# Kernel tuning notes

Measured on AMD Instinct MI355X. Metric: run time of the kernel, lower is better.

Reference implementation:

```python
import jax, jax.numpy as jnp
import numpy as np

B, T, E, H = 32, 256, 512, 512


def setup_inputs() -> dict:
    key = jax.random.key(0)
    ks = jax.random.split(key, 9)
    s_e = 1.0 / np.sqrt(E)  # nn.Linear default init bound
    s_h = 1.0 / np.sqrt(H)

    def u(k, shape, s):
        return jax.random.uniform(k, shape, jnp.float32, -s, s)

    # Gate order along the 4H axis: [in, forget, cell, out]
    return {
        "x": jax.random.normal(ks[0], (B, T, E), jnp.float32),
        "fwd_Wih": u(ks[1], (E, 4 * H), s_e),
        "fwd_bih": u(ks[2], (4 * H,), s_e),
        "fwd_Whh": u(ks[3], (H, 4 * H), s_h),
        "fwd_bhh": u(ks[4], (4 * H,), s_h),
        "bwd_Wih": u(ks[5], (E, 4 * H), s_e),
        "bwd_bih": u(ks[6], (4 * H,), s_e),
        "bwd_Whh": u(ks[7], (H, 4 * H), s_h),
        "bwd_bhh": u(ks[8], (4 * H,), s_h),
    }


def _lstm(x_seq, Wih, bih, Whh, bhh):
    """Run one LSTM direction over x_seq [B,T,E]; returns hidden states [B,T,H]
    in scan order (no flipping), matching the torch loop."""
    b, h = x_seq.shape[0], Whh.shape[0]
    # Precompute all input projections (and fold both biases) in one big GEMM.
    xg = jnp.einsum("bte,eg->tbg", x_seq, Wih) + bih + bhh  # [T,B,4H]
    h0 = jnp.zeros((b, h), x_seq.dtype)
    c0 = jnp.zeros((b, h), x_seq.dtype)

    def step(carry, xg_t):
        hprev, cprev = carry
        g = xg_t + hprev @ Whh  # [B,4H]
        i, f, gc, o = jnp.split(g, 4, axis=-1)
        c = jax.nn.sigmoid(f) * cprev + jax.nn.sigmoid(i) * jnp.tanh(gc)
        hnew = jax.nn.sigmoid(o) * jnp.tanh(c)
        return (hnew, c), hnew

    _, hs = jax.lax.scan(step, (h0, c0), xg)  # hs: [T,B,H]
    return hs.transpose(1, 0, 2)


def reference(x, fwd_Wih, fwd_bih, fwd_Whh, fwd_bhh,
              bwd_Wih, bwd_bih, bwd_Whh, bwd_bhh):
    fwd = _lstm(x, fwd_Wih, fwd_bih, fwd_Whh, fwd_bhh)
    # Backward direction processes reversed inputs; outputs are stacked in
    # processing order (the torch module does NOT re-flip them).
    bwd = _lstm(x[:, ::-1, :], bwd_Wih, bwd_bih, bwd_Whh, bwd_bhh)
    return jnp.concatenate([fwd, bwd], axis=-1)  # [B,T,2H]
```

## Files before the change

kernel.cpp:

```cpp
#include <hip/hip_runtime.h>
#include <hip/hip_bf16.h>
#include <math.h>

static constexpr int BB = 32;
static constexpr int TT = 256;
static constexpr int EE = 512;
static constexpr int HH = 512;
static constexpr int GG = 2048;

static constexpr int HS2 = 12;

using u16 = unsigned short;

__device__ __forceinline__ float bf2f(u16 u) {
    return __uint_as_float(((unsigned int)u) << 16);
}
__device__ __forceinline__ u16 f2bf(float f) {
    unsigned int u = __float_as_uint(f);
    unsigned int r = 0x7FFFu + ((u >> 16) & 1u);
    return (u16)((u + r) >> 16);
}
__device__ __forceinline__ float sigm(float x) {
    return 1.0f / (1.0f + expf(-x));
}

__device__ __forceinline__ float4 ld_b128_sc(const float4* p) {
    float4 v;
    asm volatile("global_load_dwordx4 %0, %1, off sc0 sc1" : "=v"(v) : "v"(p));
    return v;
}
__device__ __forceinline__ void st_b32_sc(float* p, float v) {
    asm volatile("global_store_dword %0, %1, off sc0 sc1" :: "v"(p), "v"(v) : "memory");
}

template<bool F32>
__device__ __forceinline__ float ldw(const void* p, size_t i) {
    if constexpr (F32) return ((const float*)p)[i];
    else               return bf2f(((const u16*)p)[i]);
}
template<bool F32>
__device__ __forceinline__ float4 ld4(const void* p, size_t i) {
    if constexpr (F32) {
        return *(const float4*)((const float*)p + i);
    } else {
        ushort4 v = *(const ushort4*)((const u16*)p + i);
        return make_float4(bf2f(v.x), bf2f(v.y), bf2f(v.z), bf2f(v.w));
    }
}

__global__ void init_state(const u16* __restrict__ bih_probe,
                           float* __restrict__ h_st, float* __restrict__ c_st,
                           int* __restrict__ bar, int* __restrict__ flag) {
    size_t i = (size_t)blockIdx.x * blockDim.x + threadIdx.x;
    size_t stride = (size_t)gridDim.x * blockDim.x;
    for (size_t j = i; j < (size_t)2*2*BB*HH; j += stride) h_st[j] = 0.0f;
    for (size_t j = i; j < (size_t)2*BB*HH;   j += stride) c_st[j] = 0.0f;
    for (size_t j = i; j < 1024;              j += stride) bar[j] = 0;
    if (blockIdx.x == 0 && threadIdx.x == 0) {
        int f = 0;
        for (int k = 0; k < 2048; ++k) {
            int e = (bih_probe[k] >> 7) & 0xFF;
            if (e >= 127) f = 1;
        }
        *flag = f;
    }
}

template<bool F32>
__device__ __forceinline__ void xg_body(
    const void* __restrict__ x, const void* __restrict__ Wih,
    const void* __restrict__ bih, const void* __restrict__ bhh,
    float* __restrict__ xgp, int d, int mt, int nt, float* b_lds)
{
    const int tid = threadIdx.x;
    const int tn = tid & 15;
    const int tm = tid >> 4;
    const int m0 = mt * 64;
    const int n0 = nt * 64;

    size_t a_off[4];
    #pragma unroll
    for (int i = 0; i < 4; ++i) {
        const int m = m0 + 4*tm + i;
        const int t = m >> 5, b = m & 31;
        const int t_src = d ? (TT - 1 - t) : t;
        a_off[i] = ((size_t)b * TT + t_src) * EE;
    }

    float acc[4][4];
    #pragma unroll
    for (int i = 0; i < 4; ++i)
        #pragma unroll
        for (int j = 0; j < 4; ++j) acc[i][j] = 0.0f;

    const int kr = tid >> 2;
    const int nc = (tid & 3) * 16;

    for (int k0 = 0; k0 < EE; k0 += 64) {
        __syncthreads();
        #pragma unroll 4
        for (int e = 0; e < 16; ++e)
            b_lds[kr*64 + nc + e] = ldw<F32>(Wih, (size_t)(k0 + kr)*GG + n0 + nc + e);
        __syncthreads();

        #pragma unroll 2
        for (int kk = 0; kk < 64; kk += 4) {
            float4 av[4];
            #pragma unroll
            for (int i = 0; i < 4; ++i) av[i] = ld4<F32>(x, a_off[i] + k0 + kk);
            #pragma unroll
            for (int j = 0; j < 4; ++j) {
                const float4 bv = *(const float4*)&b_lds[(kk + j)*64 + 4*tn];
                #pragma unroll
                for (int i = 0; i < 4; ++i) {
                    const float a = (j == 0) ? av[i].x : (j == 1) ? av[i].y
                                  : (j == 2) ? av[i].z : av[i].w;
                    acc[i][0] += a * bv.x; acc[i][1] += a * bv.y;
                    acc[i][2] += a * bv.z; acc[i][3] += a * bv.w;
                }
            }
        }
    }

    const int mbase = m0 + 4*tm;
    const int tt = mbase >> 5, bb = mbase & 31;
    #pragma unroll
    for (int j = 0; j < 4; ++j) {
        const int col  = n0 + 4*tn + j;
        const float bs = ldw<F32>(bih, col) + ldw<F32>(bhh, col);
        const int g    = col >> 9;
        const int hc   = col & 511;
        const int wgc  = hc >> 4;
        const int hcl  = hc & 15;
        const int bg8  = bb >> 3;
        const int brem = bb & 7;
        const size_t idx = (((size_t)d*TT + tt)*65536)
                         + (size_t)bg8*16384 + (size_t)wgc*512
                         + (size_t)(hcl*4 + g)*8 + brem;
        float4 v = make_float4(acc[0][j] + bs, acc[1][j] + bs,
                               acc[2][j] + bs, acc[3][j] + bs);
        *(float4*)&xgp[idx] = v;
    }
}

__global__ __launch_bounds__(256) void xg_gemm(
    const void* __restrict__ x,
    const void* __restrict__ WihF, const void* __restrict__ bihF, const void* __restrict__ bhhF,
    const void* __restrict__ WihB, const void* __restrict__ bihB, const void* __restrict__ bhhB,
    float* __restrict__ xgp, const int* __restrict__ flag)
{
    __shared__ float b_lds[64 * 64];
    const int bid = blockIdx.x;
    const int d  = bid >> 12;
    const int r  = bid & 4095;
    const int mt = r >> 5;
    const int nt = r & 31;
    const void* Wih = d ? WihB : WihF;
    const void* bih = d ? bihB : bihF;
    const void* bhh = d ? bhhB : bhhF;
    if (*flag) xg_body<true >(x, Wih, bih, bhh, xgp, d, mt, nt, b_lds);
    else       xg_body<false>(x, Wih, bih, bhh, xgp, d, mt, nt, b_lds);
}

template<bool F32>
__device__ __forceinline__ void rec_body(
    const void* __restrict__ Whh,
    const float* __restrict__ xgp,
    float* __restrict__ hT,
    int* __restrict__ bar,
    void* __restrict__ out, int d, int bg8, int wgc,
    float* __restrict__ w_lds,
    float* __restrict__ h_lds,
    float* __restrict__ gbuf)
{
    const int tid = threadIdx.x;
    const int kg = tid & 7;
    const int bq = (tid >> 3) & 1;
    const int cq = tid >> 4;

    {
        const int c  = tid & 63;
        const int kq = tid >> 6;
        const int gcol = (c & 3)*512 + wgc*16 + (c >> 2);
        char* wb = (char*)w_lds;
        for (int k = kq*128; k < kq*128 + 128; ++k) {
            const unsigned byte = (unsigned)(k*256 + c*4) ^ ((unsigned)(k & 7) << 4);
            *(float*)(wb + byte) = ldw<F32>(Whh, (size_t)k*GG + gcol);
        }
    }

    const int ch = d*4 + bg8;
    int* barc = bar + ch*128;
    float* hTc = hT + (size_t)ch * 8192;

    float cr = 0.0f;
    const int ghcl = tid >> 3;
    const int gb   = tid & 7;

    const char* wpB = (const char*)w_lds + kg*256 + ((unsigned)(cq*16) ^ ((unsigned)kg << 4));
    const float* hp = h_lds + kg*HS2 + bq*4;

    __syncthreads();

    for (int t = 0; t < TT; ++t) {
        const int parity = t & 1;
        const float4* hprev4 = (const float4*)(hTc + (parity ^ 1) * 4096);
        float*        hnext  = hTc + parity * 4096;

        float xgv[4] = {0.f, 0.f, 0.f, 0.f};
        if (tid < 128) {
            const float* xgs = xgp + (((size_t)d*TT + t)*65536)
                             + (size_t)bg8*16384 + (size_t)wgc*512;
            #pragma unroll
            for (int g = 0; g < 4; ++g)
                xgv[g] = xgs[(ghcl*4 + g)*8 + gb];
        }

        float4 hstg[4];
        #pragma unroll
        for (int i = 0; i < 4; ++i)
            hstg[i] = ld_b128_sc(hprev4 + i*256 + tid);
        asm volatile("s_waitcnt vmcnt(0)" ::: "memory");
        __builtin_amdgcn_sched_barrier(0);
        #pragma unroll
        for (int i = 0; i < 4; ++i) {
            const int idx = i*256 + tid;
            const int k  = idx >> 1;
            const int b4 = idx & 1;
            *(float4*)&h_lds[k*HS2 + b4*4] = hstg[i];
        }
        __syncthreads();

        float acc[4][4];
        #pragma unroll
        for (int i = 0; i < 4; ++i)
            #pragma unroll
            for (int j = 0; j < 4; ++j) acc[i][j] = 0.0f;
        #pragma unroll 8
        for (int kk = 0; kk < 64; ++kk) {
            const float4 wv = *(const float4*)(wpB + kk*2048);
            const float4 hv = *(const float4*)(hp + kk*(8*HS2));
            acc[0][0] += wv.x*hv.x; acc[0][1] += wv.x*hv.y; acc[0][2] += wv.x*hv.z; acc[0][3] += wv.x*hv.w;
            acc[1][0] += wv.y*hv.x; acc[1][1] += wv.y*hv.y; acc[1][2] += wv.y*hv.z; acc[1][3] += wv.y*hv.w;
            acc[2][0] += wv.z*hv.x; acc[2][1] += wv.z*hv.y; acc[2][2] += wv.z*hv.z; acc[2][3] += wv.z*hv.w;
            acc[3][0] += wv.w*hv.x; acc[3][1] += wv.w*hv.y; acc[3][2] += wv.w*hv.z; acc[3][3] += wv.w*hv.w;
        }

        #pragma unroll
        for (int i = 0; i < 4; ++i)
            #pragma unroll
            for (int j = 0; j < 4; ++j) {
                float v = acc[i][j];
                v += __shfl_xor(v, 1);
                v += __shfl_xor(v, 2);
                v += __shfl_xor(v, 4);
                acc[i][j] = v;
            }
        if (kg < 4) {
            const int ci = kg;
            *(float4*)&gbuf[(cq*4 + ci)*8 + bq*4] =
                make_float4(acc[ci][0], acc[ci][1], acc[ci][2], acc[ci][3]);
        }
        __syncthreads();

        if (tid < 128) {
            const float gi = gbuf[(ghcl*4 + 0)*8 + gb] + xgv[0];
            const float gf = gbuf[(ghcl*4 + 1)*8 + gb] + xgv[1];
            const float gc = gbuf[(ghcl*4 + 2)*8 + gb] + xgv[2];
            const float go = gbuf[(ghcl*4 + 3)*8 + gb] + xgv[3];
            const float cn = sigm(gf)*cr + sigm(gi)*tanhf(gc);
            cr = cn;
            const float hv = sigm(go)*tanhf(cn);
            const int hc = wgc*16 + ghcl;
            st_b32_sc(hnext + (size_t)hc*8 + gb, hv);
            const int bglob = bg8*8 + gb;
            const size_t oi = ((size_t)bglob*TT + t)*(2*HH) + (size_t)d*HH + hc;
            if constexpr (F32) ((float*)out)[oi] = hv;
            else               ((u16*)out)[oi]   = f2bf(hv);
        }

        asm volatile("s_waitcnt vmcnt(0)" ::: "memory");
        __syncthreads();
        if (tid == 0) {
            __hip_atomic_fetch_add(barc, 1, __ATOMIC_RELAXED, __HIP_MEMORY_SCOPE_AGENT);
            const int tgt = 32 * (t + 1);
            while (__hip_atomic_load(barc, __ATOMIC_RELAXED, __HIP_MEMORY_SCOPE_AGENT) < tgt)
                __builtin_amdgcn_s_sleep(1);
        }
        __syncthreads();
    }
}

__global__ __launch_bounds__(256, 1) void lstm_rec(
    const void* __restrict__ WhhF, const void* __restrict__ WhhB,
    const float* __restrict__ xgp, float* __restrict__ hT,
    int* __restrict__ bar, const int* __restrict__ flag,
    void* __restrict__ out)
{
    __shared__ float w_lds[512 * 64];
    __shared__ float h_lds[512 * HS2];
    __shared__ float gbuf[512];
    const int wg  = blockIdx.x;
    const int d   = wg >> 7;
    const int r   = wg & 127;
    const int bg8 = r >> 5;
    const int wgc = r & 31;
    const void* Whh = d ? WhhB : WhhF;
    if (*flag) rec_body<true >(Whh, xgp, hT, bar, out, d, bg8, wgc, w_lds, h_lds, gbuf);
    else       rec_body<false>(Whh, xgp, hT, bar, out, d, bg8, wgc, w_lds, h_lds, gbuf);
}

template<bool F32>
__device__ __forceinline__ void step_body(
    const void* __restrict__ x,
    const void* __restrict__ Wih, const void* __restrict__ bih,
    const void* __restrict__ Whh, const void* __restrict__ bhh,
    const float* __restrict__ h_prev, float* __restrict__ h_next,
    float* __restrict__ c_st, void* __restrict__ out,
    int d, int nblk, int t, int t_src, float* __restrict__ gbuf)
{
    const int tid = threadIdx.x;
    const int c0  = tid & 15;
    const int g   = c0 >> 2;
    const int nl  = c0 & 3;
    const int bq  = tid >> 4;
    const int col = g*512 + nblk*4 + nl;
    const int b0 = bq*2, b1 = b0 + 1;

    float p00=0.f,p01=0.f,p02=0.f,p03=0.f;
    float p10=0.f,p11=0.f,p12=0.f,p13=0.f;
    {
        const size_t xo0 = ((size_t)b0*TT + t_src) * EE;
        const size_t xo1 = ((size_t)b1*TT + t_src) * EE;
        #pragma unroll 4
        for (int k = 0; k < EE; k += 4) {
            const size_t wi = (size_t)k*GG + col;
            float w0 = ldw<F32>(Wih, wi);
            float w1 = ldw<F32>(Wih, wi +   (size_t)GG);
            float w2 = ldw<F32>(Wih, wi + 2*(size_t)GG);
            float w3 = ldw<F32>(Wih, wi + 3*(size_t)GG);
            float4 a0 = ld4<F32>(x, xo0 + k);
            float4 a1 = ld4<F32>(x, xo1 + k);
            p00 += w0*a0.x; p01 += w1*a0.y; p02 += w2*a0.z; p03 += w3*a0.w;
            p10 += w0*a1.x; p11 += w1*a1.y; p12 += w2*a1.z; p13 += w3*a1.w;
        }
    }
    {
        const float* hr0 = h_prev + (size_t)b0*HH;
        const float* hr1 = h_prev + (size_t)b1*HH;
        #pragma unroll 4
        for (int k = 0; k < HH; k += 4) {
            const size_t wi = (size_t)k*GG + col;
            float w0 = ldw<F32>(Whh, wi);
            float w1 = ldw<F32>(Whh, wi +   (size_t)GG);
            float w2 = ldw<F32>(Whh, wi + 2*(size_t)GG);
            float w3 = ldw<F32>(Whh, wi + 3*(size_t)GG);
            float4 v0 = *(const float4*)(hr0 + k);
            float4 v1 = *(const float4*)(hr1 + k);
            p00 += w0*v0.x; p01 += w1*v0.y; p02 += w2*v0.z; p03 += w3*v0.w;
            p10 += w0*v1.x; p11 += w1*v1.y; p12 += w2*v1.z; p13 += w3*v1.w;
        }
    }
    const float bias = ldw<F32>(bih, col) + ldw<F32>(bhh, col);
    gbuf[tid*2 + 0] = p00 + p01 + p02 + p03 + bias;
    gbuf[tid*2 + 1] = p10 + p11 + p12 + p13 + bias;
    __syncthreads();
    if (c0 < 4) {
        const int nlc = c0;
        const int ng  = nblk*4 + nlc;
        #pragma unroll
        for (int bi = 0; bi < 2; ++bi) {
            const int b = bq*2 + bi;
            const float gi = gbuf[(bq*16 + 0  + nlc)*2 + bi];
            const float gf = gbuf[(bq*16 + 4  + nlc)*2 + bi];
            const float gc = gbuf[(bq*16 + 8  + nlc)*2 + bi];
            const float go = gbuf[(bq*16 + 12 + nlc)*2 + bi];
            const size_t ci = (size_t)b*HH + ng;
            const float cp = c_st[ci];
            const float cn = sigm(gf)*cp + sigm(gi)*tanhf(gc);
            c_st[ci] = cn;
            const float hv = sigm(go)*tanhf(cn);
            h_next[ci] = hv;
            const size_t oi = ((size_t)b*TT + t)*(2*HH) + (size_t)d*HH + ng;
            if constexpr (F32) ((float*)out)[oi] = hv;
            else               ((u16*)out)[oi]   = f2bf(hv);
        }
    }
}

__global__ __launch_bounds__(256) void lstm_step(
    const void* __restrict__ x,
    const void* __restrict__ WihF, const void* __restrict__ bihF,
    const void* __restrict__ WhhF, const void* __restrict__ bhhF,
    const void* __restrict__ WihB, const void* __restrict__ bihB,
    const void* __restrict__ WhhB, const void* __restrict__ bhhB,
    float* __restrict__ h_buf, float* __restrict__ c_buf,
    const int* __restrict__ flag, void* __restrict__ out, int t)
{
    __shared__ float gbuf[512];
    const int bid  = blockIdx.x;
    const int d    = bid >> 7;
    const int nblk = bid & 127;
    const void* Wih = d ? WihB : WihF;
    const void* Whh = d ? WhhB : WhhF;
    const void* bih = d ? bihB : bihF;
    const void* bhh = d ? bhhB : bhhF;
    const int t_src  = d ? (TT - 1 - t) : t;
    const int parity = t & 1;
    const float* h_prev = h_buf + ((size_t)(d*2 + (parity ^ 1))) * BB * HH;
    float*       h_next = h_buf + ((size_t)(d*2 + parity)) * BB * HH;
    float*       c_st   = c_buf + (size_t)d * BB * HH;
    if (*flag) step_body<true >(x, Wih, bih, Whh, bhh, h_prev, h_next, c_st, out, d, nblk, t, t_src, gbuf);
    else       step_body<false>(x, Wih, bih, Whh, bhh, h_prev, h_next, c_st, out, d, nblk, t, t_src, gbuf);
}

extern "C" void kernel_launch(void* const* d_in, const int* in_sizes, int n_in,
                              void* d_out, int out_size, void* d_ws, size_t ws_size,
                              hipStream_t stream) {
    const void* x    = d_in[0];
    const void* WihF = d_in[1];
    const void* bihF = d_in[2];
    const void* WhhF = d_in[3];
    const void* bhhF = d_in[4];
    const void* WihB = d_in[5];
    const void* bihB = d_in[6];
    const void* WhhB = d_in[7];
    const void* bhhB = d_in[8];

    float* ws = (float*)d_ws;

    const size_t off_xg = 0;
    const size_t off_h  = (size_t)2*TT*BB*GG;
    const size_t off_c  = off_h + (size_t)2*2*BB*HH;
    const size_t off_b  = off_c + (size_t)2*BB*HH;
    const size_t off_f  = off_b + 1024;
    const size_t need_bytes = (off_f + 16) * sizeof(float);

    if (ws_size >= need_bytes) {
        float* xgp  = ws + off_xg;
        float* hT   = ws + off_h;
        float* cbuf = ws + off_c;
        int*   bar  = (int*)(ws + off_b);
        int*   flag = (int*)(ws + off_f);

        init_state<<<64, 256, 0, stream>>>((const u16*)bihF, hT, cbuf, bar, flag);
        xg_gemm<<<8192, 256, 0, stream>>>(x, WihF, bihF, bhhF, WihB, bihB, bhhB, xgp, flag);
        lstm_rec<<<256, 256, 0, stream>>>(WhhF, WhhB, xgp, hT, bar, flag, d_out);
    } else {
        float* h_buf = ws;
        float* c_buf = ws + (size_t)2*2*BB*HH;
        int*   bar   = (int*)(c_buf + (size_t)2*BB*HH);
        int*   flag  = (int*)(bar + 1024);
        init_state<<<64, 256, 0, stream>>>((const u16*)bihF, h_buf, c_buf, bar, flag);
        for (int t = 0; t < TT; ++t) {
            lstm_step<<<256, 256, 0, stream>>>(x, WihF, bihF, WhhF, bhhF,
                                               WihB, bihB, WhhB, bhhB,
                                               h_buf, c_buf, flag, d_out, t);
        }
    }
}
```

Before: 2.262 ms.

## Add per-tile readiness counters so recurrence can overlap the input-projection GEMM

The xg GEMM now walks time tiles in order and, after each tile's coherent stores, bumps a per-(direction, time-tile) counter. The recurrent kernel waits on these counters just before it needs each tile, instead of relying on the whole GEMM having finished. The aim is to let the serial recurrence start while the projection GEMM is still running. Both kernels are still launched on the same stream, so the GEMM will likely finish before the recurrence starts and nothing overlaps. What remains is extra atomics, spin checks and cache-bypassing stores.

```diff
diff --git a/kernel.cpp b/kernel.cpp
--- a/kernel.cpp
+++ b/kernel.cpp
@@ -11,6 +11,7 @@
 static constexpr int HS2 = 12;
 
 using u16 = unsigned short;
+typedef float f32x4 __attribute__((ext_vector_type(4)));
 
 __device__ __forceinline__ float bf2f(u16 u) {
     return __uint_as_float(((unsigned int)u) << 16);
@@ -25,12 +26,16 @@
 }
 
 __device__ __forceinline__ float4 ld_b128_sc(const float4* p) {
-    float4 v;
+    f32x4 v;
     asm volatile("global_load_dwordx4 %0, %1, off sc0 sc1" : "=v"(v) : "v"(p));
-    return v;
+    return make_float4(v.x, v.y, v.z, v.w);
 }
 __device__ __forceinline__ void st_b32_sc(float* p, float v) {
     asm volatile("global_store_dword %0, %1, off sc0 sc1" :: "v"(p), "v"(v) : "memory");
+}
+__device__ __forceinline__ void st_b128_sc(float* p, float4 v) {
+    f32x4 vv = {v.x, v.y, v.z, v.w};
+    asm volatile("global_store_dwordx4 %0, %1, off sc0 sc1" :: "v"(p), "v"(vv) : "memory");
 }
 
 template<bool F32>
@@ -55,7 +60,7 @@
     size_t stride = (size_t)gridDim.x * blockDim.x;
     for (size_t j = i; j < (size_t)2*2*BB*HH; j += stride) h_st[j] = 0.0f;
     for (size_t j = i; j < (size_t)2*BB*HH;   j += stride) c_st[j] = 0.0f;
-    for (size_t j = i; j < 1024;              j += stride) bar[j] = 0;
+    for (size_t j = i; j < 2048;              j += stride) bar[j] = 0;
     if (blockIdx.x == 0 && threadIdx.x == 0) {
         int f = 0;
         for (int k = 0; k < 2048; ++k) {
@@ -139,7 +144,7 @@
                          + (size_t)(hcl*4 + g)*8 + brem;
         float4 v = make_float4(acc[0][j] + bs, acc[1][j] + bs,
                                acc[2][j] + bs, acc[3][j] + bs);
-        *(float4*)&xgp[idx] = v;
+        st_b128_sc(&xgp[idx], v);
     }
 }
 
@@ -147,19 +152,24 @@
     const void* __restrict__ x,
     const void* __restrict__ WihF, const void* __restrict__ bihF, const void* __restrict__ bhhF,
     const void* __restrict__ WihB, const void* __restrict__ bihB, const void* __restrict__ bhhB,
-    float* __restrict__ xgp, const int* __restrict__ flag)
+    float* __restrict__ xgp, const int* __restrict__ flag,
+    int* __restrict__ xgr)
 {
     __shared__ float b_lds[64 * 64];
     const int bid = blockIdx.x;
-    const int d  = bid >> 12;
-    const int r  = bid & 4095;
-    const int mt = r >> 5;
-    const int nt = r & 31;
+    const int mt = bid >> 6;
+    const int d  = (bid >> 5) & 1;
+    const int nt = bid & 31;
     const void* Wih = d ? WihB : WihF;
     const void* bih = d ? bihB : bihF;
     const void* bhh = d ? bhhB : bhhF;
     if (*flag) xg_body<true >(x, Wih, bih, bhh, xgp, d, mt, nt, b_lds);
     else       xg_body<false>(x, Wih, bih, bhh, xgp, d, mt, nt, b_lds);
+    asm volatile("s_waitcnt vmcnt(0)" ::: "memory");
+    __syncthreads();
+    if (threadIdx.x == 0)
+        __hip_atomic_fetch_add(&xgr[d*128 + mt], 1,
+                               __ATOMIC_RELAXED, __HIP_MEMORY_SCOPE_AGENT);
 }
 
 template<bool F32>
@@ -168,6 +178,7 @@
     const float* __restrict__ xgp,
     float* __restrict__ hT,
     int* __restrict__ bar,
+    int* __restrict__ xgr,
     void* __restrict__ out, int d, int bg8, int wgc,
     float* __restrict__ w_lds,
     float* __restrict__ h_lds,
@@ -191,6 +202,7 @@
 
     const int ch = d*4 + bg8;
     int* barc = bar + ch*128;
+    int* xrd  = xgr + d*128;
     float* hTc = hT + (size_t)ch * 8192;
 
     float cr = 0.0f;
@@ -200,6 +212,11 @@
     const char* wpB = (const char*)w_lds + kg*256 + ((unsigned)(cq*16) ^ ((unsigned)kg << 4));
     const float* hp = h_lds + kg*HS2 + bq*4;
 
+    int mtDone = 1;
+    if (tid == 0) {
+        while (__hip_atomic_load(&xrd[0], __ATOMIC_RELAXED, __HIP_MEMORY_SCOPE_AGENT) < 32)
+            __builtin_amdgcn_s_sleep(1);
+    }
     __syncthreads();
 
     for (int t = 0; t < TT; ++t) {
@@ -286,6 +303,12 @@
             const int tgt = 32 * (t + 1);
             while (__hip_atomic_load(barc, __ATOMIC_RELAXED, __HIP_MEMORY_SCOPE_AGENT) < tgt)
                 __builtin_amdgcn_s_sleep(1);
+            const int mtn = (t + 1) >> 1;
+            if (mtn >= mtDone && mtn < 128) {
+                while (__hip_atomic_load(&xrd[mtn], __ATOMIC_RELAXED, __HIP_MEMORY_SCOPE_AGENT) < 32)
+                    __builtin_amdgcn_s_sleep(1);
+                mtDone = mtn + 1;
+            }
         }
         __syncthreads();
     }
@@ -294,8 +317,8 @@
 __global__ __launch_bounds__(256, 1) void lstm_rec(
     const void* __restrict__ WhhF, const void* __restrict__ WhhB,
     const float* __restrict__ xgp, float* __restrict__ hT,
-    int* __restrict__ bar, const int* __restrict__ flag,
-    void* __restrict__ out)
+    int* __restrict__ bar, int* __restrict__ xgr,
+    const int* __restrict__ flag, void* __restrict__ out)
 {
     __shared__ float w_lds[512 * 64];
     __shared__ float h_lds[512 * HS2];
@@ -306,8 +329,8 @@
     const int bg8 = r >> 5;
     const int wgc = r & 31;
     const void* Whh = d ? WhhB : WhhF;
-    if (*flag) rec_body<true >(Whh, xgp, hT, bar, out, d, bg8, wgc, w_lds, h_lds, gbuf);
-    else       rec_body<false>(Whh, xgp, hT, bar, out, d, bg8, wgc, w_lds, h_lds, gbuf);
+    if (*flag) rec_body<true >(Whh, xgp, hT, bar, xgr, out, d, bg8, wgc, w_lds, h_lds, gbuf);
+    else       rec_body<false>(Whh, xgp, hT, bar, xgr, out, d, bg8, wgc, w_lds, h_lds, gbuf);
 }
 
 template<bool F32>
@@ -433,7 +456,7 @@
     const size_t off_h  = (size_t)2*TT*BB*GG;
     const size_t off_c  = off_h + (size_t)2*2*BB*HH;
     const size_t off_b  = off_c + (size_t)2*BB*HH;
-    const size_t off_f  = off_b + 1024;
+    const size_t off_f  = off_b + 2048;
     const size_t need_bytes = (off_f + 16) * sizeof(float);
 
     if (ws_size >= need_bytes) {
@@ -441,11 +464,12 @@
         float* hT   = ws + off_h;
         float* cbuf = ws + off_c;
         int*   bar  = (int*)(ws + off_b);
+        int*   xgr  = bar + 1536;
         int*   flag = (int*)(ws + off_f);
 
         init_state<<<64, 256, 0, stream>>>((const u16*)bihF, hT, cbuf, bar, flag);
-        xg_gemm<<<8192, 256, 0, stream>>>(x, WihF, bihF, bhhF, WihB, bihB, bhhB, xgp, flag);
-        lstm_rec<<<256, 256, 0, stream>>>(WhhF, WhhB, xgp, hT, bar, flag, d_out);
+        xg_gemm<<<8192, 256, 0, stream>>>(x, WihF, bihF, bhhF, WihB, bihB, bhhB, xgp, flag, xgr);
+        lstm_rec<<<256, 256, 0, stream>>>(WhhF, WhhB, xgp, hT, bar, xgr, flag, d_out);
     } else {
         float* h_buf = ws;
         float* c_buf = ws + (size_t)2*2*BB*HH;
```

After: 2.200 ms. 1.03x faster.
